# Performance work log

Hardware: AMD Instinct MI355X
Metric: run time of the kernel (lower is better)

The kernel has to match this reference:

```python
import jax, jax.numpy as jnp
import numpy as np

GRID_SIZE, K, NUM_EXPERTS = 5, 3, 8
N_MLP, N_KAN = 4, 4
B, D, H, O = 4096, 512, 2048, 512


def _bspline_basis(x, grid, k):
    """Cox-de Boor recursion, vectorized. x: [B, D]; grid: [G]. Returns [B, D, G-k-1]."""
    xe = x[..., None]
    # order-0: indicator of grid interval
    b = ((grid[:-1] <= xe) & (xe < grid[1:])).astype(x.dtype)  # [B, D, G-1]
    for kk in range(1, k + 1):
        t_i = grid[: -(kk + 1)]
        t_ik = grid[kk:-1]
        t_ik1 = grid[kk + 1:]
        t_i1 = grid[1:-kk]
        left = (xe - t_i) / (t_ik - t_i) * b[..., :-1]
        right = (t_ik1 - xe) / (t_ik1 - t_i1) * b[..., 1:]
        b = left + right
    return b


def setup_inputs() -> dict:
    key = jax.random.key(0)
    ks = jax.random.split(key, 8)
    x = jax.random.normal(ks[0], (B, D), dtype=jnp.float32)
    # Router output: binary expert mask; rows with no active group fall back to expert 7
    mask = (jax.random.uniform(ks[1], (B, NUM_EXPERTS)) < 0.3).astype(jnp.float32)
    other = jnp.zeros((NUM_EXPERTS,), jnp.float32).at[7].set(1.0)
    expert_mask = jnp.where(mask.sum(axis=1, keepdims=True) == 0, other[None, :], mask)
    s_d = 1.0 / np.sqrt(D)
    s_h = 1.0 / np.sqrt(H)
    gate_w = jax.random.normal(ks[2], (D, NUM_EXPERTS), jnp.float32) * s_d
    gate_b = jnp.zeros((NUM_EXPERTS,), jnp.float32)
    mlp_w1 = jax.random.normal(ks[3], (N_MLP, D, H), jnp.float32) * s_d
    mlp_b1 = jnp.zeros((N_MLP, H), jnp.float32)
    mlp_w2 = jax.random.normal(ks[4], (N_MLP, H, O), jnp.float32) * s_h
    mlp_b2 = jnp.zeros((N_MLP, O), jnp.float32)
    kan_scaling = jnp.ones((N_KAN, D, O), jnp.float32)
    kan_coeff = jax.random.normal(ks[5], (N_KAN, D, O, GRID_SIZE + K), jnp.float32)
    return dict(x=x, expert_mask=expert_mask, gate_w=gate_w, gate_b=gate_b,
                mlp_w1=mlp_w1, mlp_b1=mlp_b1, mlp_w2=mlp_w2, mlp_b2=mlp_b2,
                kan_scaling=kan_scaling, kan_coeff=kan_coeff)


def reference(x, expert_mask, gate_w, gate_b, mlp_w1, mlp_b1, mlp_w2, mlp_b2,
              kan_scaling, kan_coeff):
    # gate softmax + router mask + renormalize
    gate = jax.nn.softmax(x @ gate_w + gate_b, axis=1)          # [B, E]
    masked = gate * expert_mask
    w = masked / (masked.sum(axis=1, keepdims=True) + 1e-9)      # [B, E]

    # MLP experts (eval mode -> dropout is identity)
    h = jax.nn.relu(jnp.einsum('bd,edh->ebh', x, mlp_w1) + mlp_b1[:, None, :])
    mlp_out = jnp.einsum('ebh,eho->ebo', h, mlp_w2) + mlp_b2[:, None, :]  # [4, B, O]

    # KAN experts: uniform grid extended by k knots each side (spacing 2/grid_size)
    hg = 2.0 / GRID_SIZE
    grid = jnp.arange(GRID_SIZE + 2 * K + 1, dtype=x.dtype) * hg - (1.0 + K * hg)
    basis = _bspline_basis(x, grid, K)                           # [B, D, 8]
    ceff = kan_coeff * kan_scaling[..., None]                    # [4, D, O, 8]
    kan_out = jnp.einsum('big,eiog->ebo', basis, ceff)           # [4, B, O]

    expert_outputs = jnp.concatenate([mlp_out, kan_out], axis=0)  # [8, B, O]
    out = jnp.einsum('ebo,be->bo', expert_outputs, w)             # [B, O]
    return out, expert_mask, w
```

## Files before the change

kernel.cpp:

```cpp
#include <hip/hip_runtime.h>

typedef __attribute__((ext_vector_type(4))) float f32x4;
typedef __attribute__((ext_vector_type(8))) __bf16 bf16x8;
typedef __attribute__((ext_vector_type(4))) unsigned short u16x4;
typedef __attribute__((ext_vector_type(8))) unsigned short u16x8;

#define NB 4096
#define ND 512
#define NH 2048
#define NO 512

__device__ __forceinline__ unsigned short f2bf(float f) {
  unsigned int u = __float_as_uint(f);
  u += 0x7fffu + ((u >> 16) & 1u);
  return (unsigned short)(u >> 16);
}
__device__ __forceinline__ float bf2f(unsigned short u) {
  return __uint_as_float(((unsigned int)u) << 16);
}
__device__ __forceinline__ void gload_lds16(const void* g, void* l) {
  __builtin_amdgcn_global_load_lds(
      (const __attribute__((address_space(1))) unsigned int*)g,
      (__attribute__((address_space(3))) unsigned int*)l, 16, 0, 0);
}

__global__ void gate_kernel(const float* __restrict__ x, const float* __restrict__ emask,
                            const float* __restrict__ gw, const float* __restrict__ gb,
                            float* __restrict__ w_out, float* __restrict__ mask_out) {
  int b = blockIdx.x;
  int lane = threadIdx.x;
  float l8[8] = {0,0,0,0,0,0,0,0};
  const float* xr = x + (size_t)b * ND;
  for (int d = lane; d < ND; d += 64) {
    float xv = xr[d];
    const float* g = gw + d * 8;
#pragma unroll
    for (int e = 0; e < 8; ++e) l8[e] = fmaf(xv, g[e], l8[e]);
  }
#pragma unroll
  for (int off = 32; off > 0; off >>= 1) {
#pragma unroll
    for (int e = 0; e < 8; ++e) l8[e] += __shfl_xor(l8[e], off);
  }
  float m = -1e30f;
#pragma unroll
  for (int e = 0; e < 8; ++e) { l8[e] += gb[e]; m = fmaxf(m, l8[e]); }
  float s = 0.f, p[8];
#pragma unroll
  for (int e = 0; e < 8; ++e) { p[e] = expf(l8[e] - m); s += p[e]; }
  float inv = 1.f / s;
  float mk[8], me[8], ms = 0.f;
#pragma unroll
  for (int e = 0; e < 8; ++e) {
    mk[e] = emask[(size_t)b * 8 + e];
    me[e] = p[e] * inv * mk[e];
    ms += me[e];
  }
  float winv = 1.f / (ms + 1e-9f);
  if (lane == 0) {
#pragma unroll
    for (int e = 0; e < 8; ++e) {
      w_out[(size_t)b * 8 + e] = me[e] * winv;
      mask_out[(size_t)b * 8 + e] = mk[e];
    }
  }
}

__global__ void cast_x_kernel(const float* __restrict__ x, unsigned short* __restrict__ xb) {
  size_t i = ((size_t)blockIdx.x * 256 + threadIdx.x) * 4;
  f32x4 v = *(const f32x4*)(x + i);
  u16x4 r;
#pragma unroll
  for (int j = 0; j < 4; ++j) r[j] = f2bf(v[j]);
  *(u16x4*)(xb + i) = r;
}

__global__ void basis_kernel(const float* __restrict__ x, unsigned short* __restrict__ bas) {
  size_t t = (size_t)blockIdx.x * 256 + threadIdx.x;
  float xv = x[t];
  const float hg = 0.4f;
  float tt[12];
#pragma unroll
  for (int j = 0; j < 12; ++j) tt[j] = -2.2f + hg * (float)j;
  float b0[11];
#pragma unroll
  for (int j = 0; j < 11; ++j) b0[j] = (tt[j] <= xv && xv < tt[j + 1]) ? 1.f : 0.f;
  float b1[10], b2[9], b3[8];
#pragma unroll
  for (int j = 0; j < 10; ++j) b1[j] = ((xv - tt[j]) * b0[j] + (tt[j + 2] - xv) * b0[j + 1]) * (1.f / (1.f * hg));
#pragma unroll
  for (int j = 0; j < 9; ++j)  b2[j] = ((xv - tt[j]) * b1[j] + (tt[j + 3] - xv) * b1[j + 1]) * (1.f / (2.f * hg));
#pragma unroll
  for (int j = 0; j < 8; ++j)  b3[j] = ((xv - tt[j]) * b2[j] + (tt[j + 4] - xv) * b2[j + 1]) * (1.f / (3.f * hg));
  u16x8 r;
#pragma unroll
  for (int j = 0; j < 8; ++j) r[j] = f2bf(b3[j]);
  *(u16x8*)(bas + t * 8) = r;
}

__global__ void transpose_cast(const float* __restrict__ in, unsigned short* __restrict__ outp,
                               int R, int Cc) {
  __shared__ float tile[32][33];
  int e = blockIdx.z;
  int c0 = blockIdx.x * 32, r0 = blockIdx.y * 32;
  int tx = threadIdx.x & 31, ty = threadIdx.x >> 5;
  const float* ine = in + (size_t)e * R * Cc;
  unsigned short* oute = outp + (size_t)e * R * Cc;
#pragma unroll
  for (int j = 0; j < 32; j += 8)
    tile[ty + j][tx] = ine[(size_t)(r0 + ty + j) * Cc + (c0 + tx)];
  __syncthreads();
#pragma unroll
  for (int j = 0; j < 32; j += 8)
    oute[(size_t)(c0 + ty + j) * R + (r0 + tx)] = f2bf(tile[tx][ty + j]);
}

__global__ void make_cefft(const float* __restrict__ coeff, const float* __restrict__ scal,
                           unsigned short* __restrict__ outp) {
  size_t t = (size_t)blockIdx.x * 256 + threadIdx.x;
  int i = (int)(t & 511);
  int o = (int)((t >> 9) & 511);
  int e = (int)(t >> 18);
  size_t io = ((size_t)e * 512 + i) * 512 + o;
  const f32x4* cp = (const f32x4*)(coeff + io * 8);
  f32x4 c0 = cp[0], c1 = cp[1];
  float s = scal[io];
  u16x8 r;
#pragma unroll
  for (int j = 0; j < 4; ++j) r[j] = f2bf(c0[j] * s);
#pragma unroll
  for (int j = 0; j < 4; ++j) r[4 + j] = f2bf(c1[j] * s);
  *(u16x8*)(outp + ((size_t)e * 512 + o) * 4096 + (size_t)i * 8) = r;
}

template <int MODE>
__global__ __launch_bounds__(256, 3) void gemm_bt(
    const unsigned short* __restrict__ A, size_t strideAe, int lda,
    const unsigned short* __restrict__ Bm, size_t strideBe, int ldb,
    const float* __restrict__ bias, int strideBiasE,
    unsigned short* __restrict__ C, size_t strideCe, int ldc, int K) {
  __shared__ __align__(16) char lsA[3 * 8192];
  __shared__ __align__(16) char lsB[3 * 8192];
  const int tid = threadIdx.x;
  const int lane = tid & 63, wid = tid >> 6;
  const int wr = wid >> 1, wc = wid & 1;
  const int gx = gridDim.x;
  const int nxy = gx * gridDim.y;
  int flat = blockIdx.y * gx + blockIdx.x;
  flat = (flat & 7) * (nxy >> 3) + (flat >> 3);
  const int brow = (flat / gx) * 128, bcol = (flat % gx) * 128;
  const int e = blockIdx.z;
  const unsigned short* Ae = A + (size_t)e * strideAe;
  const unsigned short* Be = Bm + (size_t)e * strideBe;
  const int NT = K >> 5;

  const int fr = lane & 15, fc = lane >> 4;
  const int sR = tid >> 2, ssc = tid & 3;

  auto stage = [&](int buf, int t2) {
#pragma unroll
    for (int q = 0; q < 2; ++q) {
      int R = q * 64 + sR;
      int kk = t2 * 32 + ((ssc ^ ((R >> 1) & 3)) << 3);
      gload_lds16(Ae + (size_t)(brow + R) * lda + (size_t)kk,
                  lsA + buf * 8192 + q * 4096 + tid * 16);
    }
#pragma unroll
    for (int q = 0; q < 2; ++q) {
      int R = q * 64 + sR;
      int kk = t2 * 32 + ((ssc ^ ((R >> 1) & 3)) << 3);
      gload_lds16(Be + (size_t)(bcol + R) * ldb + (size_t)kk,
                  lsB + buf * 8192 + q * 4096 + tid * 16);
    }
  };

  f32x4 acc[4][4] = {};

  stage(0, 0);
  stage(1, 1);
  asm volatile("s_waitcnt vmcnt(4)" ::: "memory");
  __builtin_amdgcn_s_barrier();

  int bi = 0;
  for (int t = 0; t < NT; ++t) {
    const char* bA = lsA + bi * 8192;
    const char* bB = lsB + bi * 8192;
    const int pb = (bi == 0) ? 2 : bi - 1;
    const bool pf = (t + 2 < NT);

    bf16x8 af[4], bfrag[4];
#pragma unroll
    for (int i = 0; i < 4; ++i) {
      int ra = wr * 64 + i * 16 + fr;
      af[i] = *(const bf16x8*)(bA + ra * 64 + ((fc ^ ((ra >> 1) & 3)) << 4));
      int rb = wc * 64 + i * 16 + fr;
      bfrag[i] = *(const bf16x8*)(bB + rb * 64 + ((fc ^ ((rb >> 1) & 3)) << 4));
    }
    if (pf) stage(pb, t + 2);
    __builtin_amdgcn_s_barrier();
    asm volatile("s_waitcnt lgkmcnt(0)" ::: "memory");
    __builtin_amdgcn_sched_barrier(0);
    __builtin_amdgcn_s_setprio(1);
#pragma unroll
    for (int mi = 0; mi < 4; ++mi)
#pragma unroll
      for (int ni = 0; ni < 4; ++ni)
        acc[mi][ni] = __builtin_amdgcn_mfma_f32_16x16x32_bf16(bfrag[ni], af[mi], acc[mi][ni], 0, 0, 0);
    __builtin_amdgcn_s_setprio(0);
    if (pf)               asm volatile("s_waitcnt vmcnt(4)" ::: "memory");
    else if (t + 1 < NT)  asm volatile("s_waitcnt vmcnt(0)" ::: "memory");
    __builtin_amdgcn_s_barrier();

    bi = (bi == 2) ? 0 : bi + 1;
  }

  unsigned short* Ce = C + (size_t)e * strideCe;
#pragma unroll
  for (int mi = 0; mi < 4; ++mi) {
    int row = brow + wr * 64 + mi * 16 + fr;
#pragma unroll
    for (int ni = 0; ni < 4; ++ni) {
      int col0 = bcol + wc * 64 + ni * 16 + (fc << 2);
      f32x4 bv = {0.f, 0.f, 0.f, 0.f};
      if constexpr (MODE != 2) bv = *(const f32x4*)(bias + e * strideBiasE + col0);
      u16x4 r;
#pragma unroll
      for (int j = 0; j < 4; ++j) {
        float v = acc[mi][ni][j] + bv[j];
        if constexpr (MODE == 0) v = fmaxf(v, 0.f);
        r[j] = f2bf(v);
      }
      *(u16x4*)(Ce + (size_t)row * ldc + col0) = r;
    }
  }
}

__global__ void combine_kernel(const unsigned short* __restrict__ eo,
                               const float* __restrict__ w, float* __restrict__ out) {
  int b = blockIdx.x;
  int o = threadIdx.x * 4;
  float wv[8];
#pragma unroll
  for (int e = 0; e < 8; ++e) wv[e] = w[(size_t)b * 8 + e];
  f32x4 acc = {0.f, 0.f, 0.f, 0.f};
#pragma unroll
  for (int e = 0; e < 8; ++e) {
    u16x4 u = *(const u16x4*)(eo + ((size_t)e * NB + b) * NO + o);
#pragma unroll
    for (int j = 0; j < 4; ++j) acc[j] = fmaf(wv[e], bf2f(u[j]), acc[j]);
  }
  *(f32x4*)(out + (size_t)b * NO + o) = acc;
}

extern "C" void kernel_launch(void* const* d_in, const int* in_sizes, int n_in,
                              void* d_out, int out_size, void* d_ws, size_t ws_size,
                              hipStream_t stream) {
  (void)in_sizes; (void)n_in; (void)out_size; (void)ws_size;
  const float* x      = (const float*)d_in[0];
  const float* emask  = (const float*)d_in[1];
  const float* gate_w = (const float*)d_in[2];
  const float* gate_b = (const float*)d_in[3];
  const float* mlp_w1 = (const float*)d_in[4];
  const float* mlp_b1 = (const float*)d_in[5];
  const float* mlp_w2 = (const float*)d_in[6];
  const float* mlp_b2 = (const float*)d_in[7];
  const float* kan_s  = (const float*)d_in[8];
  const float* kan_c  = (const float*)d_in[9];

  float* out = (float*)d_out;
  float* mask_out = out + (size_t)NB * NO;
  float* w_out    = mask_out + (size_t)NB * 8;

  char* ws = (char*)d_ws;
  size_t off = 0;
  auto take = [&](size_t bytes) { size_t r = off; off += (bytes + 255) & ~(size_t)255; return r; };
  unsigned short* w1t   = (unsigned short*)(ws + take((size_t)4 * NH * ND * 2));
  unsigned short* w2t   = (unsigned short*)(ws + take((size_t)4 * NO * NH * 2));
  unsigned short* cefft = (unsigned short*)(ws + take((size_t)4 * NO * (ND * 8) * 2));
  unsigned short* xbf   = (unsigned short*)(ws + take((size_t)NB * ND * 2));
  unsigned short* eo    = (unsigned short*)(ws + take((size_t)8 * NB * NO * 2));
  unsigned short* hbuf  = (unsigned short*)(ws + take((size_t)4 * NB * NH * 2));
  unsigned short* bas   = hbuf;

  gate_kernel<<<NB, 64, 0, stream>>>(x, emask, gate_w, gate_b, w_out, mask_out);
  cast_x_kernel<<<(NB * ND) / (256 * 4), 256, 0, stream>>>(x, xbf);
  transpose_cast<<<dim3(NH / 32, ND / 32, 4), 256, 0, stream>>>(mlp_w1, w1t, ND, NH);
  transpose_cast<<<dim3(NO / 32, NH / 32, 4), 256, 0, stream>>>(mlp_w2, w2t, NH, NO);
  make_cefft<<<(4 * ND * NO) / 256, 256, 0, stream>>>(kan_c, kan_s, cefft);

  gemm_bt<0><<<dim3(NH / 128, NB / 128, 4), 256, 0, stream>>>(
      xbf, 0, ND,
      w1t, (size_t)NH * ND, ND,
      mlp_b1, NH,
      hbuf, (size_t)NB * NH, NH, ND);
  gemm_bt<1><<<dim3(NO / 128, NB / 128, 4), 256, 0, stream>>>(
      hbuf, (size_t)NB * NH, NH,
      w2t, (size_t)NO * NH, NH,
      mlp_b2, NO,
      eo, (size_t)NB * NO, NO, NH);
  basis_kernel<<<(NB * ND) / 256, 256, 0, stream>>>(x, bas);
  gemm_bt<2><<<dim3(NO / 128, NB / 128, 4), 256, 0, stream>>>(
      bas, 0, ND * 8,
      cefft, (size_t)NO * (ND * 8), ND * 8,
      nullptr, 0,
      eo + (size_t)4 * NB * NO, (size_t)NB * NO, NO, ND * 8);

  combine_kernel<<<NB, NO / 4, 0, stream>>>(eo, w_out, out);
}
```

Before: 242.9 us.

## Use 256x256 GEMM tiles with 512 threads and split-K halves for second-stage GEMMs

Each GEMM block now computes a 256x256 output tile with 8 waves instead of 128x128 with 4, doubling LDS buffers and accumulator registers to raise arithmetic intensity per loaded byte. The down-projection and KAN GEMMs are split in two along K, writing partial bf16 outputs that the combine kernel sums, with the MLP second bias moved into combine. This keeps enough blocks to fill the GPU with the larger tiles, but costs more register pressure, lower occupancy, and bf16 rounding of each partial sum.

```diff
diff --git a/kernel.cpp b/kernel.cpp
--- a/kernel.cpp
+++ b/kernel.cpp
@@ -134,25 +134,28 @@
 }
 
 template <int MODE>
-__global__ __launch_bounds__(256, 3) void gemm_bt(
+__global__ __launch_bounds__(512, 2) void gemm_bt(
     const unsigned short* __restrict__ A, size_t strideAe, int lda,
     const unsigned short* __restrict__ Bm, size_t strideBe, int ldb,
     const float* __restrict__ bias, int strideBiasE,
-    unsigned short* __restrict__ C, size_t strideCe, int ldc, int K) {
-  __shared__ __align__(16) char lsA[3 * 8192];
-  __shared__ __align__(16) char lsB[3 * 8192];
+    unsigned short* __restrict__ C, size_t strideCe, size_t strideHalf, int ldc,
+    int Kspan, int zshift) {
+  __shared__ __align__(16) char lsA[3 * 16384];
+  __shared__ __align__(16) char lsB[3 * 16384];
   const int tid = threadIdx.x;
   const int lane = tid & 63, wid = tid >> 6;
-  const int wr = wid >> 1, wc = wid & 1;
+  const int wr = wid >> 2, wc = wid & 3;
   const int gx = gridDim.x;
   const int nxy = gx * gridDim.y;
   int flat = blockIdx.y * gx + blockIdx.x;
   flat = (flat & 7) * (nxy >> 3) + (flat >> 3);
-  const int brow = (flat / gx) * 128, bcol = (flat % gx) * 128;
-  const int e = blockIdx.z;
-  const unsigned short* Ae = A + (size_t)e * strideAe;
-  const unsigned short* Be = Bm + (size_t)e * strideBe;
-  const int NT = K >> 5;
+  const int brow = (flat / gx) * 256, bcol = (flat % gx) * 256;
+  const int z = blockIdx.z;
+  const int e = z >> zshift;
+  const int half = z & ((1 << zshift) - 1);
+  const unsigned short* Ae = A + (size_t)e * strideAe + (size_t)half * Kspan;
+  const unsigned short* Be = Bm + (size_t)e * strideBe + (size_t)half * Kspan;
+  const int NT = Kspan >> 5;
 
   const int fr = lane & 15, fc = lane >> 4;
   const int sR = tid >> 2, ssc = tid & 3;
@@ -160,21 +163,21 @@
   auto stage = [&](int buf, int t2) {
 #pragma unroll
     for (int q = 0; q < 2; ++q) {
-      int R = q * 64 + sR;
+      int R = q * 128 + sR;
       int kk = t2 * 32 + ((ssc ^ ((R >> 1) & 3)) << 3);
       gload_lds16(Ae + (size_t)(brow + R) * lda + (size_t)kk,
-                  lsA + buf * 8192 + q * 4096 + tid * 16);
+                  lsA + buf * 16384 + q * 8192 + tid * 16);
     }
 #pragma unroll
     for (int q = 0; q < 2; ++q) {
-      int R = q * 64 + sR;
+      int R = q * 128 + sR;
       int kk = t2 * 32 + ((ssc ^ ((R >> 1) & 3)) << 3);
       gload_lds16(Be + (size_t)(bcol + R) * ldb + (size_t)kk,
-                  lsB + buf * 8192 + q * 4096 + tid * 16);
+                  lsB + buf * 16384 + q * 8192 + tid * 16);
     }
   };
 
-  f32x4 acc[4][4] = {};
+  f32x4 acc[8][4] = {};
 
   stage(0, 0);
   stage(1, 1);
@@ -183,18 +186,21 @@
 
   int bi = 0;
   for (int t = 0; t < NT; ++t) {
-    const char* bA = lsA + bi * 8192;
-    const char* bB = lsB + bi * 8192;
+    const char* bA = lsA + bi * 16384;
+    const char* bB = lsB + bi * 16384;
     const int pb = (bi == 0) ? 2 : bi - 1;
     const bool pf = (t + 2 < NT);
 
-    bf16x8 af[4], bfrag[4];
-#pragma unroll
-    for (int i = 0; i < 4; ++i) {
-      int ra = wr * 64 + i * 16 + fr;
+    bf16x8 af[8], bfrag[4];
+#pragma unroll
+    for (int i = 0; i < 8; ++i) {
+      int ra = wr * 128 + i * 16 + fr;
       af[i] = *(const bf16x8*)(bA + ra * 64 + ((fc ^ ((ra >> 1) & 3)) << 4));
-      int rb = wc * 64 + i * 16 + fr;
-      bfrag[i] = *(const bf16x8*)(bB + rb * 64 + ((fc ^ ((rb >> 1) & 3)) << 4));
+    }
+#pragma unroll
+    for (int n = 0; n < 4; ++n) {
+      int rb = wc * 64 + n * 16 + fr;
+      bfrag[n] = *(const bf16x8*)(bB + rb * 64 + ((fc ^ ((rb >> 1) & 3)) << 4));
     }
     if (pf) stage(pb, t + 2);
     __builtin_amdgcn_s_barrier();
@@ -202,7 +208,7 @@
     __builtin_amdgcn_sched_barrier(0);
     __builtin_amdgcn_s_setprio(1);
 #pragma unroll
-    for (int mi = 0; mi < 4; ++mi)
+    for (int mi = 0; mi < 8; ++mi)
 #pragma unroll
       for (int ni = 0; ni < 4; ++ni)
         acc[mi][ni] = __builtin_amdgcn_mfma_f32_16x16x32_bf16(bfrag[ni], af[mi], acc[mi][ni], 0, 0, 0);
@@ -214,28 +220,30 @@
     bi = (bi == 2) ? 0 : bi + 1;
   }
 
-  unsigned short* Ce = C + (size_t)e * strideCe;
-#pragma unroll
-  for (int mi = 0; mi < 4; ++mi) {
-    int row = brow + wr * 64 + mi * 16 + fr;
+  unsigned short* Ce = C + (size_t)e * strideCe + (size_t)half * strideHalf;
+#pragma unroll
+  for (int mi = 0; mi < 8; ++mi) {
+    int row = brow + wr * 128 + mi * 16 + fr;
 #pragma unroll
     for (int ni = 0; ni < 4; ++ni) {
       int col0 = bcol + wc * 64 + ni * 16 + (fc << 2);
-      f32x4 bv = {0.f, 0.f, 0.f, 0.f};
-      if constexpr (MODE != 2) bv = *(const f32x4*)(bias + e * strideBiasE + col0);
       u16x4 r;
-#pragma unroll
-      for (int j = 0; j < 4; ++j) {
-        float v = acc[mi][ni][j] + bv[j];
-        if constexpr (MODE == 0) v = fmaxf(v, 0.f);
-        r[j] = f2bf(v);
+      if constexpr (MODE == 0) {
+        f32x4 bv = *(const f32x4*)(bias + e * strideBiasE + col0);
+#pragma unroll
+        for (int j = 0; j < 4; ++j) r[j] = f2bf(fmaxf(acc[mi][ni][j] + bv[j], 0.f));
+      } else {
+#pragma unroll
+        for (int j = 0; j < 4; ++j) r[j] = f2bf(acc[mi][ni][j]);
       }
       *(u16x4*)(Ce + (size_t)row * ldc + col0) = r;
     }
   }
 }
 
-__global__ void combine_kernel(const unsigned short* __restrict__ eo,
+__global__ void combine_kernel(const unsigned short* __restrict__ eoM,
+                               const unsigned short* __restrict__ eoK,
+                               const float* __restrict__ b2,
                                const float* __restrict__ w, float* __restrict__ out) {
   int b = blockIdx.x;
   int o = threadIdx.x * 4;
@@ -244,10 +252,21 @@
   for (int e = 0; e < 8; ++e) wv[e] = w[(size_t)b * 8 + e];
   f32x4 acc = {0.f, 0.f, 0.f, 0.f};
 #pragma unroll
-  for (int e = 0; e < 8; ++e) {
-    u16x4 u = *(const u16x4*)(eo + ((size_t)e * NB + b) * NO + o);
-#pragma unroll
-    for (int j = 0; j < 4; ++j) acc[j] = fmaf(wv[e], bf2f(u[j]), acc[j]);
+  for (int e = 0; e < 4; ++e) {
+    u16x4 m0 = *(const u16x4*)(eoM + ((size_t)e * NB + b) * NO + o);
+    u16x4 m1 = *(const u16x4*)(eoM + ((size_t)(4 + e) * NB + b) * NO + o);
+    f32x4 bb = *(const f32x4*)(b2 + e * NO + o);
+#pragma unroll
+    for (int j = 0; j < 4; ++j)
+      acc[j] = fmaf(wv[e], bf2f(m0[j]) + bf2f(m1[j]) + bb[j], acc[j]);
+  }
+#pragma unroll
+  for (int e = 0; e < 4; ++e) {
+    u16x4 k0 = *(const u16x4*)(eoK + ((size_t)e * NB + b) * NO + o);
+    u16x4 k1 = *(const u16x4*)(eoK + ((size_t)(4 + e) * NB + b) * NO + o);
+#pragma unroll
+    for (int j = 0; j < 4; ++j)
+      acc[j] = fmaf(wv[4 + e], bf2f(k0[j]) + bf2f(k1[j]), acc[j]);
   }
   *(f32x4*)(out + (size_t)b * NO + o) = acc;
 }
@@ -278,9 +297,10 @@
   unsigned short* w2t   = (unsigned short*)(ws + take((size_t)4 * NO * NH * 2));
   unsigned short* cefft = (unsigned short*)(ws + take((size_t)4 * NO * (ND * 8) * 2));
   unsigned short* xbf   = (unsigned short*)(ws + take((size_t)NB * ND * 2));
-  unsigned short* eo    = (unsigned short*)(ws + take((size_t)8 * NB * NO * 2));
+  unsigned short* eoM   = (unsigned short*)(ws + take((size_t)8 * NB * NO * 2));
   unsigned short* hbuf  = (unsigned short*)(ws + take((size_t)4 * NB * NH * 2));
   unsigned short* bas   = hbuf;
+  unsigned short* eoK   = (unsigned short*)((char*)hbuf + (size_t)2 * NB * NH * 2);
 
   gate_kernel<<<NB, 64, 0, stream>>>(x, emask, gate_w, gate_b, w_out, mask_out);
   cast_x_kernel<<<(NB * ND) / (256 * 4), 256, 0, stream>>>(x, xbf);
@@ -288,22 +308,22 @@
   transpose_cast<<<dim3(NO / 32, NH / 32, 4), 256, 0, stream>>>(mlp_w2, w2t, NH, NO);
   make_cefft<<<(4 * ND * NO) / 256, 256, 0, stream>>>(kan_c, kan_s, cefft);
 
-  gemm_bt<0><<<dim3(NH / 128, NB / 128, 4), 256, 0, stream>>>(
+  gemm_bt<0><<<dim3(NH / 256, NB / 256, 4), 512, 0, stream>>>(
       xbf, 0, ND,
       w1t, (size_t)NH * ND, ND,
       mlp_b1, NH,
-      hbuf, (size_t)NB * NH, NH, ND);
-  gemm_bt<1><<<dim3(NO / 128, NB / 128, 4), 256, 0, stream>>>(
+      hbuf, (size_t)NB * NH, 0, NH, ND, 0);
+  gemm_bt<2><<<dim3(NO / 256, NB / 256, 8), 512, 0, stream>>>(
       hbuf, (size_t)NB * NH, NH,
       w2t, (size_t)NO * NH, NH,
-      mlp_b2, NO,
-      eo, (size_t)NB * NO, NO, NH);
+      nullptr, 0,
+      eoM, (size_t)NB * NO, (size_t)4 * NB * NO, NO, NH / 2, 1);
   basis_kernel<<<(NB * ND) / 256, 256, 0, stream>>>(x, bas);
-  gemm_bt<2><<<dim3(NO / 128, NB / 128, 4), 256, 0, stream>>>(
+  gemm_bt<2><<<dim3(NO / 256, NB / 256, 8), 512, 0, stream>>>(
       bas, 0, ND * 8,
       cefft, (size_t)NO * (ND * 8), ND * 8,
       nullptr, 0,
-      eo + (size_t)4 * NB * NO, (size_t)NB * NO, NO, ND * 8);
-
-  combine_kernel<<<NB, NO / 4, 0, stream>>>(eo, w_out, out);
-}
+      eoK, (size_t)NB * NO, (size_t)4 * NB * NO, NO, (ND * 8) / 2, 1);
+
+  combine_kernel<<<NB, NO / 4, 0, stream>>>(eoM, eoK, mlp_b2, w_out, out);
+}
```

After: 235.0 us. -3.2%, faster.
